# Optimization experiments

Measured on AMD Instinct MI355X. Metric: run time of the kernel, lower is better.

The kernel has to match this reference:

```python
import jax, jax.numpy as jnp
import numpy as np

N_USERS = 100_000
N_ITEMS = 50_000
N = N_USERS + N_ITEMS
N_LAYERS = 3
ALPHA = 0.8
D = 64
IMG_D = 4096
TXT_D = 384
N_INTER = 2_000_000  # user-item interactions; symmetric nnz = 2*N_INTER


def setup_inputs() -> dict:
    # --- build symmetric-normalized bipartite adjacency (D^-1/2 A D^-1/2) in numpy ---
    rng = np.random.default_rng(0)
    u = rng.integers(0, N_USERS, N_INTER).astype(np.int32)
    i = (rng.integers(0, N_ITEMS, N_INTER) + N_USERS).astype(np.int32)
    rows = np.concatenate([u, i])
    cols = np.concatenate([i, u])
    deg = np.bincount(rows, minlength=N).astype(np.float32)
    d_inv = np.where(deg > 0, deg ** -0.5, 0.0).astype(np.float32)
    vals = d_inv[rows] * d_inv[cols]

    key = jax.random.key(0)
    ks = jax.random.split(key, 8)
    xav_img = float(np.sqrt(6.0 / (IMG_D + D)))
    xav_txt = float(np.sqrt(6.0 / (TXT_D + D)))
    return {
        "image_feats": jax.random.normal(ks[0], (N_ITEMS, IMG_D), jnp.float32),
        "text_feats": jax.random.normal(ks[1], (N_ITEMS, TXT_D), jnp.float32),
        "image_pref": jax.random.normal(ks[2], (N_USERS, D), jnp.float32),
        "text_pref": jax.random.normal(ks[3], (N_USERS, D), jnp.float32),
        "W_img": jax.random.uniform(ks[4], (IMG_D, D), jnp.float32, -xav_img, xav_img),
        "b_img": jnp.zeros((D,), jnp.float32),
        "W_txt": jax.random.uniform(ks[5], (TXT_D, D), jnp.float32, -xav_txt, xav_txt),
        "b_txt": jnp.zeros((D,), jnp.float32),
        "adj_vals": jnp.asarray(vals),
        "adj_rows": jnp.asarray(rows),
        "adj_cols": jnp.asarray(cols),
    }


def _spmm(rows, cols, vals, x):
    # sparse COO @ dense: out[r] += vals[e] * x[cols[e]]
    return jax.ops.segment_sum(vals[:, None] * x[cols], rows, num_segments=N)


def _l2norm(x):
    # F.normalize(x, dim=1): row-wise L2 with eps clamp
    return x / jnp.clip(jnp.linalg.norm(x, axis=1, keepdims=True), 1e-12)


def reference(image_feats, text_feats, image_pref, text_pref,
              W_img, b_img, W_txt, b_txt, adj_vals, adj_rows, adj_cols):
    img = _l2norm(image_feats @ W_img + b_img)   # [n_items, D]
    txt = _l2norm(text_feats @ W_txt + b_txt)    # [n_items, D]
    ego_i = jnp.concatenate([image_pref, img], axis=0)  # [N, D]
    ego_t = jnp.concatenate([text_pref, txt], axis=0)   # [N, D]
    for _ in range(N_LAYERS):
        ego_i = _spmm(adj_rows, adj_cols, adj_vals, ego_i) + ALPHA * ego_i
        ego_t = _spmm(adj_rows, adj_cols, adj_vals, ego_t) + ALPHA * ego_t
    user_preference = jnp.concatenate([ego_i[:N_USERS], ego_t[:N_USERS]], axis=1)  # [n_users, 2D]
    items = jnp.concatenate([ego_i[N_USERS:], ego_t[N_USERS:]], axis=1)            # [n_items, 2D]
    return user_preference, items
```

## Files before the change

### kernel.cpp

```cpp
#include <hip/hip_runtime.h>
#include <hip/hip_bf16.h>

#define N_USERS 100000
#define N_ITEMS 50000
#define N_TOTAL 150000
#define NNZ     4000000
#define ALPHA_F 0.8f
#define ELL_CAP 128

#define G_SCAT 256
#define G_COPY 128
#define G_PRE  (G_SCAT + G_COPY)
#define G_GEMM 3125

typedef __attribute__((ext_vector_type(8))) short bf16x8;
typedef __attribute__((ext_vector_type(4))) float f32x4;

static __device__ __forceinline__ short f2bf(float f) {
    unsigned u = __builtin_bit_cast(unsigned, f);
    unsigned r = (u + 0x7fff + ((u >> 16) & 1)) >> 16;
    return (short)r;
}
static __device__ __forceinline__ unsigned pack_bf2(float a, float b) {
    return (unsigned)(unsigned short)f2bf(a) | ((unsigned)(unsigned short)f2bf(b) << 16);
}
static __device__ __forceinline__ float bf_lo(unsigned u) { return __uint_as_float(u << 16); }
static __device__ __forceinline__ float bf_hi(unsigned u) { return __uint_as_float(u & 0xFFFF0000u); }

static __device__ __forceinline__ void gload_lds16(const void* src, void* dst) {
    __builtin_amdgcn_global_load_lds(
        (const __attribute__((address_space(1))) unsigned*)src,
        (__attribute__((address_space(3))) unsigned*)dst, 16, 0, 0);
}


__global__ __launch_bounds__(256) void prep_kernel(const float* __restrict__ Wimg,
                                                   const float* __restrict__ Wtxt,
                                                   int* __restrict__ cnt,
                                                   short* __restrict__ Wti,
                                                   short* __restrict__ Wtt) {
    const int T0 = N_TOTAL;
    const int T1 = T0 + 4096 * 64;
    const int T2 = T1 + 384 * 64;
    int i = blockIdx.x * 256 + threadIdx.x;
    int stride = gridDim.x * 256;
    for (; i < T2; i += stride) {
        if (i < T0) {
            cnt[i] = 0;
        } else if (i < T1) {
            int idx = i - T0; int k = idx >> 6, n = idx & 63;
            Wti[(size_t)n * 4096 + k] = f2bf(Wimg[(size_t)k * 64 + n]);
        } else {
            int idx = i - T1; int k = idx >> 6, n = idx & 63;
            Wtt[(size_t)n * 384 + k] = f2bf(Wtxt[(size_t)k * 64 + n]);
        }
    }
}


__global__ __launch_bounds__(256, 4) void mega_kernel(
        const float* __restrict__ Aimg, const float* __restrict__ Atxt,
        const short* __restrict__ Wti, const short* __restrict__ Wtt,
        const float* __restrict__ bimg, const float* __restrict__ btxt,
        unsigned* __restrict__ egob,
        const int* __restrict__ rows, const int* __restrict__ cols,
        const float* __restrict__ vals, int* __restrict__ cnt, int2* __restrict__ ell,
        const float* __restrict__ img_pref, const float* __restrict__ txt_pref) {
    __shared__ __align__(16) char atile[32768];
    int b = blockIdx.x;
    int t = threadIdx.x;
    int wave = t >> 6, lane = t & 63;

    if (b < G_SCAT) {
        int i = b * 256 + t;
        int stride = G_SCAT * 256;
        for (; i < NNZ; i += stride) {
            int r = rows[i];
            int p = atomicAdd(&cnt[r], 1);
            if (p < ELL_CAP)
                ell[(size_t)r * ELL_CAP + p] = make_int2(cols[i], __float_as_int(vals[i]));
        }
        return;
    }
    if (b < G_PRE) {
        int idx = (b - G_SCAT) * 256 + t;
        int stride = G_COPY * 256;
        for (; idx < N_USERS * 16; idx += stride) {
            int row = idx >> 4, w4 = (idx & 15) << 2;
            float4 iv = *reinterpret_cast<const float4*>(&img_pref[(size_t)row * 64 + w4]);
            float4 tv = *reinterpret_cast<const float4*>(&txt_pref[(size_t)row * 64 + w4]);
            uint4 m;
            m.x = pack_bf2(iv.x, tv.x); m.y = pack_bf2(iv.y, tv.y);
            m.z = pack_bf2(iv.z, tv.z); m.w = pack_bf2(iv.w, tv.w);
            *reinterpret_cast<uint4*>(&egob[(size_t)row * 64 + w4]) = m;
        }
        return;
    }

    const int blk = b - G_PRE;
    const int row0 = blk * 16;
    const int col = lane & 15, kb = lane >> 4;

    auto stage_img = [&](int ci, int bi) {
        #pragma unroll
        for (int j = 0; j < 4; ++j) {
            int r = wave * 4 + j;
            int swz = (r & 7) << 4;
            const char* src = (const char*)Aimg + (size_t)(row0 + r) * 16384
                              + ci * 1024 + ((lane * 16) ^ swz);
            char* dst = (char*)atile + bi * 16384 + r * 1024;
            gload_lds16(src, dst);
        }
    };
    auto stage_txt1 = [&](int bi) {
        #pragma unroll
        for (int j = 0; j < 4; ++j) {
            int r = wave * 4 + j;
            int swz = (r & 7) << 4;
            const char* src = (const char*)Atxt + (size_t)(row0 + r) * 1536
                              + ((lane * 16) ^ swz);
            char* dst = (char*)atile + bi * 16384 + r * 1024;
            gload_lds16(src, dst);
        }
    };
    auto stage_txt2 = [&](int bi) {
        #pragma unroll
        for (int j = 0; j < 2; ++j) {
            int p = wave * 2 + j;
            int r = p * 2 + (lane >> 5);
            int swz = (r & 7) << 4;
            const char* src = (const char*)Atxt + (size_t)(row0 + r) * 1536
                              + 1024 + (((lane & 31) * 16) ^ swz);
            char* dst = (char*)atile + bi * 16384 + p * 1024;
            gload_lds16(src, dst);
        }
    };
    auto comp = [&](const char* base, int rstride, const short* Wt, int K, int kabs,
                    int nks, f32x4& acc) {
        const int row = col;
        const int swz = (row & 7) << 4;
        const char* ab = base + row * rstride;
        const short* wp = Wt + (size_t)(16 * wave + col) * K + kabs + kb * 8;
        for (int ks = 0; ks < nks; ++ks) {
            int lg = kb * 32 + ks * 128;
            float4 a0 = *(const float4*)(ab + (lg ^ swz));
            float4 a1 = *(const float4*)(ab + ((lg + 16) ^ swz));
            bf16x8 af;
            af[0]=f2bf(a0.x); af[1]=f2bf(a0.y); af[2]=f2bf(a0.z); af[3]=f2bf(a0.w);
            af[4]=f2bf(a1.x); af[5]=f2bf(a1.y); af[6]=f2bf(a1.z); af[7]=f2bf(a1.w);
            bf16x8 bf = *(const bf16x8*)(wp + ks * 32);
            acc = __builtin_amdgcn_mfma_f32_16x16x32_bf16(af, bf, acc, 0, 0, 0);
        }
    };

    f32x4 ai = {0.f,0.f,0.f,0.f}, at4 = {0.f,0.f,0.f,0.f};

    stage_img(0, 0);
    for (int ci = 0; ci < 16; ++ci) {
        int bi = ci & 1;
        if (ci < 15) stage_img(ci + 1, bi ^ 1);
        else         stage_txt1(bi ^ 1);
        asm volatile("s_waitcnt vmcnt(4)" ::: "memory");
        __builtin_amdgcn_s_barrier();
        __builtin_amdgcn_sched_barrier(0);
        comp((const char*)atile + bi * 16384, 1024, Wti, 4096, ci * 256, 8, ai);
        asm volatile("" ::: "memory");
        __builtin_amdgcn_s_barrier();
        __builtin_amdgcn_sched_barrier(0);
    }
    stage_txt2(1);
    asm volatile("s_waitcnt vmcnt(2)" ::: "memory");
    __builtin_amdgcn_s_barrier();
    __builtin_amdgcn_sched_barrier(0);
    comp((const char*)atile, 1024, Wtt, 384, 0, 8, at4);
    asm volatile("s_waitcnt vmcnt(0)" ::: "memory");
    __builtin_amdgcn_s_barrier();
    __builtin_amdgcn_sched_barrier(0);
    comp((const char*)atile + 16384, 512, Wtt, 384, 256, 4, at4);

    float bv_i = bimg[16 * wave + col];
    float bv_t = btxt[16 * wave + col];
    float ssi[4], sst[4];
    #pragma unroll
    for (int i = 0; i < 4; ++i) {
        ai[i] += bv_i; at4[i] += bv_t;
        ssi[i] = ai[i] * ai[i];
        sst[i] = at4[i] * at4[i];
    }
    #pragma unroll
    for (int off = 1; off < 16; off <<= 1) {
        #pragma unroll
        for (int i = 0; i < 4; ++i) {
            ssi[i] += __shfl_xor(ssi[i], off, 64);
            sst[i] += __shfl_xor(sst[i], off, 64);
        }
    }
    float* S = (float*)atile;
    __syncthreads();
    if (col == 0) {
        #pragma unroll
        for (int i = 0; i < 4; ++i) {
            S[wave * 16 + kb * 4 + i]      = ssi[i];
            S[64 + wave * 16 + kb * 4 + i] = sst[i];
        }
    }
    __syncthreads();
    unsigned* egob_items = egob + (size_t)N_USERS * 64;
    #pragma unroll
    for (int i = 0; i < 4; ++i) {
        int r = kb * 4 + i;
        float ti = S[r] + S[16 + r] + S[32 + r] + S[48 + r];
        float tt = S[64 + r] + S[80 + r] + S[96 + r] + S[112 + r];
        float rni = 1.0f / fmaxf(sqrtf(ti), 1e-12f);
        float rnt = 1.0f / fmaxf(sqrtf(tt), 1e-12f);
        egob_items[(size_t)(row0 + r) * 64 + 16 * wave + col] =
            pack_bf2(ai[i] * rni, at4[i] * rnt);
    }
}


__global__ __launch_bounds__(256) void spmm_sort_kernel(
        const int* __restrict__ cnt, int2* __restrict__ ell,
        const unsigned* __restrict__ xb, unsigned* __restrict__ outb) {
    __shared__ __align__(16) int2 srt[4][ELL_CAP];
    int wid = threadIdx.x >> 6, lane = threadIdx.x & 63;
    int row = blockIdx.x * 4 + wid;
    bool valid = row < N_TOTAL;
    int deg = 0;
    int2* base = nullptr;
    int2 e0 = make_int2(0x7FFFFFFF, 0), e1 = e0;
    if (valid) {
        deg = min(cnt[row], ELL_CAP);
        base = ell + (size_t)row * ELL_CAP;
        if (lane < deg)      e0 = base[lane];
        if (lane + 64 < deg) e1 = base[lane + 64];
    }
    #pragma unroll
    for (int k = 2; k <= 128; k <<= 1) {
        #pragma unroll
        for (int j = 64; j >= 1; j >>= 1) {
            if (j >= k) continue;
            if (j == 64) {
                if (e0.x > e1.x) { int2 tmp = e0; e0 = e1; e1 = tmp; }
            } else {
                int2 p0, p1;
                p0.x = __shfl_xor(e0.x, j, 64); p0.y = __shfl_xor(e0.y, j, 64);
                p1.x = __shfl_xor(e1.x, j, 64); p1.y = __shfl_xor(e1.y, j, 64);
                bool up0 = ((lane & k) == 0);
                bool up1 = (((lane + 64) & k) == 0);
                bool lo0 = ((lane & j) == 0);
                bool keepmin0 = (up0 == lo0);
                bool keepmin1 = (up1 == lo0);
                if (keepmin0 ? (e0.x > p0.x) : (e0.x < p0.x)) e0 = p0;
                if (keepmin1 ? (e1.x > p1.x) : (e1.x < p1.x)) e1 = p1;
            }
        }
    }
    if (valid) {
        if (lane < deg)      base[lane]      = e0;
        if (lane + 64 < deg) base[lane + 64] = e1;
    }
    srt[wid][lane] = e0;
    srt[wid][lane + 64] = e1;
    __syncthreads();
    if (!valid) return;
    unsigned sw = xb[(size_t)row * 64 + lane];
    float2 acc;
    acc.x = ALPHA_F * bf_lo(sw);
    acc.y = ALPHA_F * bf_hi(sw);
    const int2* s = srt[wid];
    int i = 0;
    for (; i + 8 <= deg; i += 8) {
        int4 p0 = *reinterpret_cast<const int4*>(s + i);
        int4 p1 = *reinterpret_cast<const int4*>(s + i + 2);
        int4 p2 = *reinterpret_cast<const int4*>(s + i + 4);
        int4 p3 = *reinterpret_cast<const int4*>(s + i + 6);
        unsigned g0 = xb[(size_t)p0.x * 64 + lane];
        unsigned g1 = xb[(size_t)p0.z * 64 + lane];
        unsigned g2 = xb[(size_t)p1.x * 64 + lane];
        unsigned g3 = xb[(size_t)p1.z * 64 + lane];
        unsigned g4 = xb[(size_t)p2.x * 64 + lane];
        unsigned g5 = xb[(size_t)p2.z * 64 + lane];
        unsigned g6 = xb[(size_t)p3.x * 64 + lane];
        unsigned g7 = xb[(size_t)p3.z * 64 + lane];
        float v0 = __int_as_float(p0.y), v1 = __int_as_float(p0.w);
        float v2 = __int_as_float(p1.y), v3 = __int_as_float(p1.w);
        float v4 = __int_as_float(p2.y), v5 = __int_as_float(p2.w);
        float v6 = __int_as_float(p3.y), v7 = __int_as_float(p3.w);
        acc.x = fmaf(v0, bf_lo(g0), acc.x); acc.y = fmaf(v0, bf_hi(g0), acc.y);
        acc.x = fmaf(v1, bf_lo(g1), acc.x); acc.y = fmaf(v1, bf_hi(g1), acc.y);
        acc.x = fmaf(v2, bf_lo(g2), acc.x); acc.y = fmaf(v2, bf_hi(g2), acc.y);
        acc.x = fmaf(v3, bf_lo(g3), acc.x); acc.y = fmaf(v3, bf_hi(g3), acc.y);
        acc.x = fmaf(v4, bf_lo(g4), acc.x); acc.y = fmaf(v4, bf_hi(g4), acc.y);
        acc.x = fmaf(v5, bf_lo(g5), acc.x); acc.y = fmaf(v5, bf_hi(g5), acc.y);
        acc.x = fmaf(v6, bf_lo(g6), acc.x); acc.y = fmaf(v6, bf_hi(g6), acc.y);
        acc.x = fmaf(v7, bf_lo(g7), acc.x); acc.y = fmaf(v7, bf_hi(g7), acc.y);
    }
    for (; i < deg; ++i) {
        int2 c = s[i];
        float v = __int_as_float(c.y);
        unsigned g = xb[(size_t)c.x * 64 + lane];
        acc.x = fmaf(v, bf_lo(g), acc.x);
        acc.y = fmaf(v, bf_hi(g), acc.y);
    }
    outb[(size_t)row * 64 + lane] = pack_bf2(acc.x, acc.y);
}


__global__ __launch_bounds__(256) void spmm_kernel(
        const int* __restrict__ cnt, const int2* __restrict__ ell,
        const unsigned* __restrict__ xb,
        float* __restrict__ out32, unsigned* __restrict__ outb) {
    int row = blockIdx.x * 4 + (threadIdx.x >> 6);
    if (row >= N_TOTAL) return;
    int lane = threadIdx.x & 63;
    unsigned sw = xb[(size_t)row * 64 + lane];
    float2 acc;
    acc.x = ALPHA_F * bf_lo(sw);
    acc.y = ALPHA_F * bf_hi(sw);
    int deg = min(cnt[row], ELL_CAP);
    const int2* base = ell + (size_t)row * ELL_CAP;
    int i = 0;
    for (; i + 8 <= deg; i += 8) {
        int4 p0 = *reinterpret_cast<const int4*>(base + i);
        int4 p1 = *reinterpret_cast<const int4*>(base + i + 2);
        int4 p2 = *reinterpret_cast<const int4*>(base + i + 4);
        int4 p3 = *reinterpret_cast<const int4*>(base + i + 6);
        unsigned g0 = xb[(size_t)p0.x * 64 + lane];
        unsigned g1 = xb[(size_t)p0.z * 64 + lane];
        unsigned g2 = xb[(size_t)p1.x * 64 + lane];
        unsigned g3 = xb[(size_t)p1.z * 64 + lane];
        unsigned g4 = xb[(size_t)p2.x * 64 + lane];
        unsigned g5 = xb[(size_t)p2.z * 64 + lane];
        unsigned g6 = xb[(size_t)p3.x * 64 + lane];
        unsigned g7 = xb[(size_t)p3.z * 64 + lane];
        float v0 = __int_as_float(p0.y), v1 = __int_as_float(p0.w);
        float v2 = __int_as_float(p1.y), v3 = __int_as_float(p1.w);
        float v4 = __int_as_float(p2.y), v5 = __int_as_float(p2.w);
        float v6 = __int_as_float(p3.y), v7 = __int_as_float(p3.w);
        acc.x = fmaf(v0, bf_lo(g0), acc.x); acc.y = fmaf(v0, bf_hi(g0), acc.y);
        acc.x = fmaf(v1, bf_lo(g1), acc.x); acc.y = fmaf(v1, bf_hi(g1), acc.y);
        acc.x = fmaf(v2, bf_lo(g2), acc.x); acc.y = fmaf(v2, bf_hi(g2), acc.y);
        acc.x = fmaf(v3, bf_lo(g3), acc.x); acc.y = fmaf(v3, bf_hi(g3), acc.y);
        acc.x = fmaf(v4, bf_lo(g4), acc.x); acc.y = fmaf(v4, bf_hi(g4), acc.y);
        acc.x = fmaf(v5, bf_lo(g5), acc.x); acc.y = fmaf(v5, bf_hi(g5), acc.y);
        acc.x = fmaf(v6, bf_lo(g6), acc.x); acc.y = fmaf(v6, bf_hi(g6), acc.y);
        acc.x = fmaf(v7, bf_lo(g7), acc.x); acc.y = fmaf(v7, bf_hi(g7), acc.y);
    }
    for (; i < deg; ++i) {
        int2 c = base[i];
        float v = __int_as_float(c.y);
        unsigned g = xb[(size_t)c.x * 64 + lane];
        acc.x = fmaf(v, bf_lo(g), acc.x);
        acc.y = fmaf(v, bf_hi(g), acc.y);
    }
    if (out32) {
        out32[(size_t)row * 128 + lane] = acc.x;
        out32[(size_t)row * 128 + 64 + lane] = acc.y;
    }
    if (outb)
        outb[(size_t)row * 64 + lane] = pack_bf2(acc.x, acc.y);
}


extern "C" void kernel_launch(void* const* d_in, const int* in_sizes, int n_in,
                              void* d_out, int out_size, void* d_ws, size_t ws_size,
                              hipStream_t stream) {
    const float* image_feats = (const float*)d_in[0];
    const float* text_feats  = (const float*)d_in[1];
    const float* image_pref  = (const float*)d_in[2];
    const float* text_pref   = (const float*)d_in[3];
    const float* W_img       = (const float*)d_in[4];
    const float* b_img       = (const float*)d_in[5];
    const float* W_txt       = (const float*)d_in[6];
    const float* b_txt       = (const float*)d_in[7];
    const float* adj_vals    = (const float*)d_in[8];
    const int*   adj_rows    = (const int*)d_in[9];
    const int*   adj_cols    = (const int*)d_in[10];

    float* out = (float*)d_out;

    char* ws = (char*)d_ws;
    size_t off = 0;
    auto alloc = [&](size_t bytes) { char* p = ws + off; off += (bytes + 255) & ~size_t(255); return p; };
    int*      cnt    = (int*)     alloc(N_TOTAL * sizeof(int));
    int2*     ell    = (int2*)    alloc((size_t)N_TOTAL * ELL_CAP * sizeof(int2));
    unsigned* m0     = (unsigned*)alloc((size_t)N_TOTAL * 64 * sizeof(unsigned));
    unsigned* m1     = (unsigned*)alloc((size_t)N_TOTAL * 64 * sizeof(unsigned));
    short*    Wt_img = (short*)   alloc((size_t)64 * 4096 * sizeof(short));
    short*    Wt_txt = (short*)   alloc((size_t)64 * 384 * sizeof(short));
    (void)ws_size; (void)out_size; (void)n_in; (void)in_sizes;

    prep_kernel<<<512, 256, 0, stream>>>(W_img, W_txt, cnt, Wt_img, Wt_txt);

    mega_kernel<<<G_PRE + G_GEMM, 256, 0, stream>>>(
        image_feats, text_feats, Wt_img, Wt_txt, b_img, b_txt, m0,
        adj_rows, adj_cols, adj_vals, cnt, ell, image_pref, text_pref);

    const int ROW_GRID = (N_TOTAL + 3) / 4;
    spmm_sort_kernel<<<ROW_GRID, 256, 0, stream>>>(cnt, ell, m0, m1);
    spmm_kernel<<<ROW_GRID, 256, 0, stream>>>(cnt, ell, m1, nullptr, m0);
    spmm_kernel<<<ROW_GRID, 256, 0, stream>>>(cnt, ell, m0, out, nullptr);
}
```

Baseline: 976.3 us.

## Replace async global-to-LDS staging with register-staged prefetch and widen scatter grid

The GEMM A-tile staging drops the global_load_lds direct-to-LDS path in favour of loading into registers one chunk ahead, then writing to swizzled LDS after compute, with a uniform 18-chunk loop that also covers the text features. The COO-to-ELL scatter gets four times more blocks and a 4-way unrolled loop so several atomics and loads are in flight at once. This trades the async LDS DMA for more registers and extra barriers, and may change occupancy and how well load latency is hidden.

```diff
diff --git a/kernel.cpp b/kernel.cpp
--- a/kernel.cpp
+++ b/kernel.cpp
@@ -8,10 +8,11 @@
 #define ALPHA_F 0.8f
 #define ELL_CAP 128
 
-#define G_SCAT 256
+#define G_SCAT 1024
 #define G_COPY 128
 #define G_PRE  (G_SCAT + G_COPY)
 #define G_GEMM 3125
+#define NC_ALL 18
 
 typedef __attribute__((ext_vector_type(8))) short bf16x8;
 typedef __attribute__((ext_vector_type(4))) float f32x4;
@@ -26,12 +27,6 @@
 }
 static __device__ __forceinline__ float bf_lo(unsigned u) { return __uint_as_float(u << 16); }
 static __device__ __forceinline__ float bf_hi(unsigned u) { return __uint_as_float(u & 0xFFFF0000u); }
-
-static __device__ __forceinline__ void gload_lds16(const void* src, void* dst) {
-    __builtin_amdgcn_global_load_lds(
-        (const __attribute__((address_space(1))) unsigned*)src,
-        (__attribute__((address_space(3))) unsigned*)dst, 16, 0, 0);
-}
 
 
 __global__ __launch_bounds__(256) void prep_kernel(const float* __restrict__ Wimg,
@@ -72,8 +67,22 @@
     int wave = t >> 6, lane = t & 63;
 
     if (b < G_SCAT) {
+        const int stride = G_SCAT * 256;
         int i = b * 256 + t;
-        int stride = G_SCAT * 256;
+        for (; i + 3 * stride < NNZ; i += 4 * stride) {
+            int r0 = rows[i],            c0 = cols[i];            float v0 = vals[i];
+            int r1 = rows[i + stride],   c1 = cols[i + stride];   float v1 = vals[i + stride];
+            int r2 = rows[i + 2*stride], c2 = cols[i + 2*stride]; float v2 = vals[i + 2*stride];
+            int r3 = rows[i + 3*stride], c3 = cols[i + 3*stride]; float v3 = vals[i + 3*stride];
+            int p0 = atomicAdd(&cnt[r0], 1);
+            int p1 = atomicAdd(&cnt[r1], 1);
+            int p2 = atomicAdd(&cnt[r2], 1);
+            int p3 = atomicAdd(&cnt[r3], 1);
+            if (p0 < ELL_CAP) ell[(size_t)r0 * ELL_CAP + p0] = make_int2(c0, __float_as_int(v0));
+            if (p1 < ELL_CAP) ell[(size_t)r1 * ELL_CAP + p1] = make_int2(c1, __float_as_int(v1));
+            if (p2 < ELL_CAP) ell[(size_t)r2 * ELL_CAP + p2] = make_int2(c2, __float_as_int(v2));
+            if (p3 < ELL_CAP) ell[(size_t)r3 * ELL_CAP + p3] = make_int2(c3, __float_as_int(v3));
+        }
         for (; i < NNZ; i += stride) {
             int r = rows[i];
             int p = atomicAdd(&cnt[r], 1);
@@ -101,45 +110,46 @@
     const int row0 = blk * 16;
     const int col = lane & 15, kb = lane >> 4;
 
-    auto stage_img = [&](int ci, int bi) {
-        #pragma unroll
-        for (int j = 0; j < 4; ++j) {
-            int r = wave * 4 + j;
-            int swz = (r & 7) << 4;
-            const char* src = (const char*)Aimg + (size_t)(row0 + r) * 16384
-                              + ci * 1024 + ((lane * 16) ^ swz);
-            char* dst = (char*)atile + bi * 16384 + r * 1024;
-            gload_lds16(src, dst);
-        }
+    f32x4 s0, s1, s2, s3;
+
+    auto ld_img = [&](int ci) {
+        const char* base = (const char*)Aimg + (size_t)row0 * 16384 + ci * 1024 + lane * 16;
+        s0 = *(const f32x4*)(base + (size_t)(0 * 4 + wave) * 16384);
+        s1 = *(const f32x4*)(base + (size_t)(1 * 4 + wave) * 16384);
+        s2 = *(const f32x4*)(base + (size_t)(2 * 4 + wave) * 16384);
+        s3 = *(const f32x4*)(base + (size_t)(3 * 4 + wave) * 16384);
+        __builtin_amdgcn_sched_barrier(0);
     };
-    auto stage_txt1 = [&](int bi) {
-        #pragma unroll
-        for (int j = 0; j < 4; ++j) {
-            int r = wave * 4 + j;
-            int swz = (r & 7) << 4;
-            const char* src = (const char*)Atxt + (size_t)(row0 + r) * 1536
-                              + ((lane * 16) ^ swz);
-            char* dst = (char*)atile + bi * 16384 + r * 1024;
-            gload_lds16(src, dst);
-        }
+    auto wr_img = [&](int bi) {
+        char* d = (char*)atile + bi * 16384;
+        int r0r = 0 * 4 + wave, r1r = 1 * 4 + wave, r2r = 2 * 4 + wave, r3r = 3 * 4 + wave;
+        *(f32x4*)(d + r0r * 1024 + ((lane * 16) ^ ((r0r & 7) << 4))) = s0;
+        *(f32x4*)(d + r1r * 1024 + ((lane * 16) ^ ((r1r & 7) << 4))) = s1;
+        *(f32x4*)(d + r2r * 1024 + ((lane * 16) ^ ((r2r & 7) << 4))) = s2;
+        *(f32x4*)(d + r3r * 1024 + ((lane * 16) ^ ((r3r & 7) << 4))) = s3;
     };
-    auto stage_txt2 = [&](int bi) {
-        #pragma unroll
-        for (int j = 0; j < 2; ++j) {
-            int p = wave * 2 + j;
-            int r = p * 2 + (lane >> 5);
-            int swz = (r & 7) << 4;
-            const char* src = (const char*)Atxt + (size_t)(row0 + r) * 1536
-                              + 1024 + (((lane & 31) * 16) ^ swz);
-            char* dst = (char*)atile + bi * 16384 + p * 1024;
-            gload_lds16(src, dst);
-        }
+    auto ld_txt = [&](int ci) {
+        int r = t >> 4, po = (t & 15) * 48;
+        const char* base = (const char*)Atxt + (size_t)(row0 + r) * 1536 + ci * 768 + po;
+        s0 = *(const f32x4*)(base);
+        s1 = *(const f32x4*)(base + 16);
+        s2 = *(const f32x4*)(base + 32);
+        __builtin_amdgcn_sched_barrier(0);
     };
-    auto comp = [&](const char* base, int rstride, const short* Wt, int K, int kabs,
-                    int nks, f32x4& acc) {
+    auto wr_txt = [&](int bi) {
+        int r = t >> 4, po = (t & 15) * 48, sw = (r & 7) << 4;
+        char* d = (char*)atile + bi * 16384 + r * 1024;
+        *(f32x4*)(d + ((po     ) ^ sw)) = s0;
+        *(f32x4*)(d + ((po + 16) ^ sw)) = s1;
+        *(f32x4*)(d + ((po + 32) ^ sw)) = s2;
+    };
+    auto ld = [&](int ci) { if (ci < 16) ld_img(ci); else ld_txt(ci - 16); };
+    auto wr = [&](int ci, int bi) { if (ci < 16) wr_img(bi); else wr_txt(bi); };
+
+    auto comp = [&](const char* base, const short* Wt, int K, int kabs, int nks, f32x4& acc) {
         const int row = col;
         const int swz = (row & 7) << 4;
-        const char* ab = base + row * rstride;
+        const char* ab = base + row * 1024;
         const short* wp = Wt + (size_t)(16 * wave + col) * K + kabs + kb * 8;
         for (int ks = 0; ks < nks; ++ks) {
             int lg = kb * 32 + ks * 128;
@@ -148,35 +158,28 @@
             bf16x8 af;
             af[0]=f2bf(a0.x); af[1]=f2bf(a0.y); af[2]=f2bf(a0.z); af[3]=f2bf(a0.w);
             af[4]=f2bf(a1.x); af[5]=f2bf(a1.y); af[6]=f2bf(a1.z); af[7]=f2bf(a1.w);
-            bf16x8 bf = *(const bf16x8*)(wp + ks * 32);
-            acc = __builtin_amdgcn_mfma_f32_16x16x32_bf16(af, bf, acc, 0, 0, 0);
+            bf16x8 bfr = *(const bf16x8*)(wp + ks * 32);
+            acc = __builtin_amdgcn_mfma_f32_16x16x32_bf16(af, bfr, acc, 0, 0, 0);
         }
     };
 
     f32x4 ai = {0.f,0.f,0.f,0.f}, at4 = {0.f,0.f,0.f,0.f};
 
-    stage_img(0, 0);
-    for (int ci = 0; ci < 16; ++ci) {
+    ld(0);
+    wr(0, 0);
+    __syncthreads();
+    ld(1);
+    for (int ci = 0; ci < NC_ALL; ++ci) {
         int bi = ci & 1;
-        if (ci < 15) stage_img(ci + 1, bi ^ 1);
-        else         stage_txt1(bi ^ 1);
-        asm volatile("s_waitcnt vmcnt(4)" ::: "memory");
-        __builtin_amdgcn_s_barrier();
-        __builtin_amdgcn_sched_barrier(0);
-        comp((const char*)atile + bi * 16384, 1024, Wti, 4096, ci * 256, 8, ai);
-        asm volatile("" ::: "memory");
-        __builtin_amdgcn_s_barrier();
-        __builtin_amdgcn_sched_barrier(0);
-    }
-    stage_txt2(1);
-    asm volatile("s_waitcnt vmcnt(2)" ::: "memory");
-    __builtin_amdgcn_s_barrier();
-    __builtin_amdgcn_sched_barrier(0);
-    comp((const char*)atile, 1024, Wtt, 384, 0, 8, at4);
-    asm volatile("s_waitcnt vmcnt(0)" ::: "memory");
-    __builtin_amdgcn_s_barrier();
-    __builtin_amdgcn_sched_barrier(0);
-    comp((const char*)atile + 16384, 512, Wtt, 384, 256, 4, at4);
+        if (ci < 16) comp((const char*)atile + bi * 16384, Wti, 4096, ci * 256, 8, ai);
+        else         comp((const char*)atile + bi * 16384, Wtt, 384, (ci - 16) * 192, 6, at4);
+        __syncthreads();
+        if (ci + 1 < NC_ALL) {
+            wr(ci + 1, bi ^ 1);
+            if (ci + 2 < NC_ALL) ld(ci + 2);
+            __syncthreads();
+        }
+    }
 
     float bv_i = bimg[16 * wave + col];
     float bv_t = btxt[16 * wave + col];
```

Result: slower. 1.084 ms (+11.0%).

## Split GEMM from scatter, stage swizzled bf16 weights in LDS per k-chunk

Applied to the files above, without the earlier changes.

Splits the fused mega kernel into a standalone GEMM kernel and a separate scatter/copy kernel, where the scatter work gets more blocks. Weights are pre-transposed into per-128-k chunks with an XOR swizzle so each chunk can be DMA-loaded into LDS alongside the A tile. This replaces the per-lane strided global weight loads. The GEMM loop now uses 35 uniform 128-wide chunks with double buffering and a smaller A tile. The cost is more LDS per block, so occupancy is lowered to 3, plus one extra kernel launch, and the GEMM no longer overlaps with the scatter.

```diff
diff --git a/kernel.cpp b/kernel.cpp
--- a/kernel.cpp
+++ b/kernel.cpp
@@ -8,10 +8,11 @@
 #define ALPHA_F 0.8f
 #define ELL_CAP 128
 
-#define G_SCAT 256
-#define G_COPY 128
-#define G_PRE  (G_SCAT + G_COPY)
+#define C_COPY 512
+#define C_SCAT 1024
 #define G_GEMM 3125
+#define NC_IMG 32
+#define NC_ALL 35
 
 typedef __attribute__((ext_vector_type(8))) short bf16x8;
 typedef __attribute__((ext_vector_type(4))) float f32x4;
@@ -37,8 +38,8 @@
 __global__ __launch_bounds__(256) void prep_kernel(const float* __restrict__ Wimg,
                                                    const float* __restrict__ Wtxt,
                                                    int* __restrict__ cnt,
-                                                   short* __restrict__ Wti,
-                                                   short* __restrict__ Wtt) {
+                                                   char* __restrict__ WtiT,
+                                                   char* __restrict__ WttT) {
     const int T0 = N_TOTAL;
     const int T1 = T0 + 4096 * 64;
     const int T2 = T1 + 384 * 64;
@@ -49,134 +50,88 @@
             cnt[i] = 0;
         } else if (i < T1) {
             int idx = i - T0; int k = idx >> 6, n = idx & 63;
-            Wti[(size_t)n * 4096 + k] = f2bf(Wimg[(size_t)k * 64 + n]);
+            int c = k >> 7, kk = k & 127;
+            *(short*)(WtiT + c * 16384 + n * 256 + ((kk * 2) ^ ((n & 7) << 4)))
+                = f2bf(Wimg[(size_t)k * 64 + n]);
         } else {
             int idx = i - T1; int k = idx >> 6, n = idx & 63;
-            Wtt[(size_t)n * 384 + k] = f2bf(Wtxt[(size_t)k * 64 + n]);
-        }
-    }
-}
-
-
-__global__ __launch_bounds__(256, 4) void mega_kernel(
+            int c = k >> 7, kk = k & 127;
+            *(short*)(WttT + c * 16384 + n * 256 + ((kk * 2) ^ ((n & 7) << 4)))
+                = f2bf(Wtxt[(size_t)k * 64 + n]);
+        }
+    }
+}
+
+
+__global__ __launch_bounds__(256, 3) void gemm_kernel(
         const float* __restrict__ Aimg, const float* __restrict__ Atxt,
-        const short* __restrict__ Wti, const short* __restrict__ Wtt,
+        const char* __restrict__ WtiT, const char* __restrict__ WttT,
         const float* __restrict__ bimg, const float* __restrict__ btxt,
-        unsigned* __restrict__ egob,
-        const int* __restrict__ rows, const int* __restrict__ cols,
-        const float* __restrict__ vals, int* __restrict__ cnt, int2* __restrict__ ell,
-        const float* __restrict__ img_pref, const float* __restrict__ txt_pref) {
-    __shared__ __align__(16) char atile[32768];
-    int b = blockIdx.x;
-    int t = threadIdx.x;
-    int wave = t >> 6, lane = t & 63;
-
-    if (b < G_SCAT) {
-        int i = b * 256 + t;
-        int stride = G_SCAT * 256;
-        for (; i < NNZ; i += stride) {
-            int r = rows[i];
-            int p = atomicAdd(&cnt[r], 1);
-            if (p < ELL_CAP)
-                ell[(size_t)r * ELL_CAP + p] = make_int2(cols[i], __float_as_int(vals[i]));
-        }
-        return;
-    }
-    if (b < G_PRE) {
-        int idx = (b - G_SCAT) * 256 + t;
-        int stride = G_COPY * 256;
-        for (; idx < N_USERS * 16; idx += stride) {
-            int row = idx >> 4, w4 = (idx & 15) << 2;
-            float4 iv = *reinterpret_cast<const float4*>(&img_pref[(size_t)row * 64 + w4]);
-            float4 tv = *reinterpret_cast<const float4*>(&txt_pref[(size_t)row * 64 + w4]);
-            uint4 m;
-            m.x = pack_bf2(iv.x, tv.x); m.y = pack_bf2(iv.y, tv.y);
-            m.z = pack_bf2(iv.z, tv.z); m.w = pack_bf2(iv.w, tv.w);
-            *reinterpret_cast<uint4*>(&egob[(size_t)row * 64 + w4]) = m;
-        }
-        return;
-    }
-
-    const int blk = b - G_PRE;
-    const int row0 = blk * 16;
+        unsigned* __restrict__ egob_items) {
+    __shared__ __align__(16) char abuf[2][8192];
+    __shared__ __align__(16) char bbuf[2][16384];
+    const int t = threadIdx.x;
+    const int wave = t >> 6, lane = t & 63;
     const int col = lane & 15, kb = lane >> 4;
-
-    auto stage_img = [&](int ci, int bi) {
-        #pragma unroll
-        for (int j = 0; j < 4; ++j) {
-            int r = wave * 4 + j;
-            int swz = (r & 7) << 4;
-            const char* src = (const char*)Aimg + (size_t)(row0 + r) * 16384
-                              + ci * 1024 + ((lane * 16) ^ swz);
-            char* dst = (char*)atile + bi * 16384 + r * 1024;
+    const int row0 = blockIdx.x * 16;
+
+    auto stage = [&](int ci, int bi) {
+        const float* A; size_t rowbytes; const char* BT; int cc;
+        if (ci < NC_IMG) { A = Aimg; rowbytes = 16384; BT = WtiT; cc = ci; }
+        else             { A = Atxt; rowbytes = 1536;  BT = WttT; cc = ci - NC_IMG; }
+        #pragma unroll
+        for (int q = 0; q < 2; ++q) {
+            int r = (q * 4 + wave) * 2 + (lane >> 5);
+            int so = ((lane & 31) * 16) ^ ((r & 7) << 4);
+            const char* src = (const char*)A + (size_t)(row0 + r) * rowbytes + cc * 512 + so;
+            char* dst = abuf[bi] + (q * 4 + wave) * 1024 + lane * 16;
             gload_lds16(src, dst);
         }
+        #pragma unroll
+        for (int q = 0; q < 4; ++q) {
+            int off = (q * 4 + wave) * 1024 + lane * 16;
+            gload_lds16(BT + (size_t)cc * 16384 + off, bbuf[bi] + off);
+        }
     };
-    auto stage_txt1 = [&](int bi) {
-        #pragma unroll
-        for (int j = 0; j < 4; ++j) {
-            int r = wave * 4 + j;
-            int swz = (r & 7) << 4;
-            const char* src = (const char*)Atxt + (size_t)(row0 + r) * 1536
-                              + ((lane * 16) ^ swz);
-            char* dst = (char*)atile + bi * 16384 + r * 1024;
-            gload_lds16(src, dst);
-        }
-    };
-    auto stage_txt2 = [&](int bi) {
-        #pragma unroll
-        for (int j = 0; j < 2; ++j) {
-            int p = wave * 2 + j;
-            int r = p * 2 + (lane >> 5);
-            int swz = (r & 7) << 4;
-            const char* src = (const char*)Atxt + (size_t)(row0 + r) * 1536
-                              + 1024 + (((lane & 31) * 16) ^ swz);
-            char* dst = (char*)atile + bi * 16384 + p * 1024;
-            gload_lds16(src, dst);
-        }
-    };
-    auto comp = [&](const char* base, int rstride, const short* Wt, int K, int kabs,
-                    int nks, f32x4& acc) {
-        const int row = col;
-        const int swz = (row & 7) << 4;
-        const char* ab = base + row * rstride;
-        const short* wp = Wt + (size_t)(16 * wave + col) * K + kabs + kb * 8;
-        for (int ks = 0; ks < nks; ++ks) {
-            int lg = kb * 32 + ks * 128;
-            float4 a0 = *(const float4*)(ab + (lg ^ swz));
-            float4 a1 = *(const float4*)(ab + ((lg + 16) ^ swz));
+
+    auto comp = [&](int bi, f32x4& acc) {
+        const int r = col;
+        const int aswz = (r & 7) << 4;
+        const char* ab = abuf[bi] + r * 512;
+        const int n = 16 * wave + col;
+        const char* bb = bbuf[bi] + n * 256;
+        const int bswz = (n & 7) << 4;
+        #pragma unroll
+        for (int ks = 0; ks < 4; ++ks) {
+            int la = ks * 128 + kb * 32;
+            float4 a0 = *(const float4*)(ab + (la ^ aswz));
+            float4 a1 = *(const float4*)(ab + ((la + 16) ^ aswz));
             bf16x8 af;
             af[0]=f2bf(a0.x); af[1]=f2bf(a0.y); af[2]=f2bf(a0.z); af[3]=f2bf(a0.w);
             af[4]=f2bf(a1.x); af[5]=f2bf(a1.y); af[6]=f2bf(a1.z); af[7]=f2bf(a1.w);
-            bf16x8 bf = *(const bf16x8*)(wp + ks * 32);
+            bf16x8 bf = *(const bf16x8*)(bb + ((ks * 64 + kb * 16) ^ bswz));
             acc = __builtin_amdgcn_mfma_f32_16x16x32_bf16(af, bf, acc, 0, 0, 0);
         }
     };
 
     f32x4 ai = {0.f,0.f,0.f,0.f}, at4 = {0.f,0.f,0.f,0.f};
 
-    stage_img(0, 0);
-    for (int ci = 0; ci < 16; ++ci) {
+    stage(0, 0);
+    for (int ci = 0; ci < NC_ALL; ++ci) {
         int bi = ci & 1;
-        if (ci < 15) stage_img(ci + 1, bi ^ 1);
-        else         stage_txt1(bi ^ 1);
-        asm volatile("s_waitcnt vmcnt(4)" ::: "memory");
+        if (ci + 1 < NC_ALL) {
+            stage(ci + 1, bi ^ 1);
+            asm volatile("s_waitcnt vmcnt(6)" ::: "memory");
+        } else {
+            asm volatile("s_waitcnt vmcnt(0)" ::: "memory");
+        }
         __builtin_amdgcn_s_barrier();
         __builtin_amdgcn_sched_barrier(0);
-        comp((const char*)atile + bi * 16384, 1024, Wti, 4096, ci * 256, 8, ai);
-        asm volatile("" ::: "memory");
+        if (ci < NC_IMG) comp(bi, ai);
+        else             comp(bi, at4);
+        __builtin_amdgcn_sched_barrier(0);
         __builtin_amdgcn_s_barrier();
-        __builtin_amdgcn_sched_barrier(0);
-    }
-    stage_txt2(1);
-    asm volatile("s_waitcnt vmcnt(2)" ::: "memory");
-    __builtin_amdgcn_s_barrier();
-    __builtin_amdgcn_sched_barrier(0);
-    comp((const char*)atile, 1024, Wtt, 384, 0, 8, at4);
-    asm volatile("s_waitcnt vmcnt(0)" ::: "memory");
-    __builtin_amdgcn_s_barrier();
-    __builtin_amdgcn_sched_barrier(0);
-    comp((const char*)atile + 16384, 512, Wtt, 384, 256, 4, at4);
+    }
 
     float bv_i = bimg[16 * wave + col];
     float bv_t = btxt[16 * wave + col];
@@ -195,7 +150,7 @@
             sst[i] += __shfl_xor(sst[i], off, 64);
         }
     }
-    float* S = (float*)atile;
+    float* S = (float*)abuf;
     __syncthreads();
     if (col == 0) {
         #pragma unroll
@@ -205,7 +160,6 @@
         }
     }
     __syncthreads();
-    unsigned* egob_items = egob + (size_t)N_USERS * 64;
     #pragma unroll
     for (int i = 0; i < 4; ++i) {
         int r = kb * 4 + i;
@@ -215,6 +169,37 @@
         float rnt = 1.0f / fmaxf(sqrtf(tt), 1e-12f);
         egob_items[(size_t)(row0 + r) * 64 + 16 * wave + col] =
             pack_bf2(ai[i] * rni, at4[i] * rnt);
+    }
+}
+
+
+__global__ __launch_bounds__(256) void scat_copy_kernel(
+        const int* __restrict__ rows, const int* __restrict__ cols,
+        const float* __restrict__ vals, int* __restrict__ cnt, int2* __restrict__ ell,
+        const float* __restrict__ img_pref, const float* __restrict__ txt_pref,
+        unsigned* __restrict__ egob) {
+    int b = blockIdx.x;
+    if (b < C_COPY) {
+        int idx = b * 256 + threadIdx.x;
+        int stride = C_COPY * 256;
+        for (; idx < N_USERS * 16; idx += stride) {
+            int row = idx >> 4, w4 = (idx & 15) << 2;
+            float4 iv = *reinterpret_cast<const float4*>(&img_pref[(size_t)row * 64 + w4]);
+            float4 tv = *reinterpret_cast<const float4*>(&txt_pref[(size_t)row * 64 + w4]);
+            uint4 m;
+            m.x = pack_bf2(iv.x, tv.x); m.y = pack_bf2(iv.y, tv.y);
+            m.z = pack_bf2(iv.z, tv.z); m.w = pack_bf2(iv.w, tv.w);
+            *reinterpret_cast<uint4*>(&egob[(size_t)row * 64 + w4]) = m;
+        }
+    } else {
+        int i = (b - C_COPY) * 256 + threadIdx.x;
+        int stride = C_SCAT * 256;
+        for (; i < NNZ; i += stride) {
+            int r = rows[i];
+            int p = atomicAdd(&cnt[r], 1);
+            if (p < ELL_CAP)
+                ell[(size_t)r * ELL_CAP + p] = make_int2(cols[i], __float_as_int(vals[i]));
+        }
     }
 }
 
@@ -383,19 +368,22 @@
     char* ws = (char*)d_ws;
     size_t off = 0;
     auto alloc = [&](size_t bytes) { char* p = ws + off; off += (bytes + 255) & ~size_t(255); return p; };
-    int*      cnt    = (int*)     alloc(N_TOTAL * sizeof(int));
-    int2*     ell    = (int2*)    alloc((size_t)N_TOTAL * ELL_CAP * sizeof(int2));
-    unsigned* m0     = (unsigned*)alloc((size_t)N_TOTAL * 64 * sizeof(unsigned));
-    unsigned* m1     = (unsigned*)alloc((size_t)N_TOTAL * 64 * sizeof(unsigned));
-    short*    Wt_img = (short*)   alloc((size_t)64 * 4096 * sizeof(short));
-    short*    Wt_txt = (short*)   alloc((size_t)64 * 384 * sizeof(short));
+    int*      cnt   = (int*)     alloc(N_TOTAL * sizeof(int));
+    int2*     ell   = (int2*)    alloc((size_t)N_TOTAL * ELL_CAP * sizeof(int2));
+    unsigned* m0    = (unsigned*)alloc((size_t)N_TOTAL * 64 * sizeof(unsigned));
+    unsigned* m1    = (unsigned*)alloc((size_t)N_TOTAL * 64 * sizeof(unsigned));
+    char*     WtiT  = (char*)    alloc((size_t)NC_IMG * 16384);
+    char*     WttT  = (char*)    alloc((size_t)3 * 16384);
     (void)ws_size; (void)out_size; (void)n_in; (void)in_sizes;
 
-    prep_kernel<<<512, 256, 0, stream>>>(W_img, W_txt, cnt, Wt_img, Wt_txt);
-
-    mega_kernel<<<G_PRE + G_GEMM, 256, 0, stream>>>(
-        image_feats, text_feats, Wt_img, Wt_txt, b_img, b_txt, m0,
-        adj_rows, adj_cols, adj_vals, cnt, ell, image_pref, text_pref);
+    prep_kernel<<<512, 256, 0, stream>>>(W_img, W_txt, cnt, WtiT, WttT);
+
+    unsigned* m0_items = m0 + (size_t)N_USERS * 64;
+    gemm_kernel<<<G_GEMM, 256, 0, stream>>>(
+        image_feats, text_feats, WtiT, WttT, b_img, b_txt, m0_items);
+
+    scat_copy_kernel<<<C_COPY + C_SCAT, 256, 0, stream>>>(
+        adj_rows, adj_cols, adj_vals, cnt, ell, image_pref, text_pref, m0);
 
     const int ROW_GRID = (N_TOTAL + 3) / 4;
     spmm_sort_kernel<<<ROW_GRID, 256, 0, stream>>>(cnt, ell, m0, m1);
```

After: 1.025 ms. 1.05x slower.
